# Kernel optimization log

Measured on AMD Instinct MI355X. Metric: run time of the kernel, lower is better.

The kernel has to match this reference:

```python
import jax, jax.numpy as jnp
import numpy as np

B = 2048          # batch
E = 32            # number of expert FCs (len(out_features_nested))
IN = 2048         # in_features
OUT = 1024        # out_features (uniform across experts)


def setup_inputs() -> dict:
    key = jax.random.key(0)
    k1, k2, k3, k4 = jax.random.split(key, 4)
    features = jax.random.normal(k1, (B, IN), dtype=jnp.float32)
    activated = jax.random.normal(k2, (B, E), dtype=jnp.float32)
    # Stacked per-expert Linear params: W[e] is [OUT, IN], b[e] is [OUT]
    W = jax.random.normal(k3, (E, OUT, IN), dtype=jnp.float32) * (1.0 / np.sqrt(IN))
    b = jax.random.normal(k4, (E, OUT), dtype=jnp.float32) * 0.01
    return {"features": features, "W": W, "b": b, "activated": activated, "top_k": 4}


def reference(features, W, b, activated, top_k):
    # Original: parent_indices = activated.argsort(dim=1)[:, :top_k]  (ascending!)
    idx = jnp.argsort(activated, axis=1)[:, :top_k]            # [B, K] int
    # Dense all-expert compute (grouped GEMM), then per-sample gather of the
    # top_k selected experts' outputs. Equivalent math to per-sample Linear calls.
    all_out = jnp.einsum('bi,eoi->beo', features, W) + b        # [B, E, OUT]
    out = jnp.take_along_axis(all_out, idx[:, :, None], axis=1)  # [B, K, OUT]
    return out
```

## Files before the change

### kernel.cpp

```cpp
#include <hip/hip_runtime.h>
#include <hip/hip_bf16.h>
#include <stdint.h>

#define B_N     2048
#define E_N     32
#define IN_N    2048
#define OUT_N   1024
#define TOPK    4

#define BM      128
#define BN      256
#define BK      32
#define NT      (OUT_N / BN)
#define NKT     (IN_N / BK)
#define THREADS 512
#define MAX_SLOTS 96
#define GRID_GEMM (MAX_SLOTS * NT)

#define WS_COUNTS 0
#define WS_NSLOTS 32
#define WS_DESC   64
#define WS_LISTS  256

typedef float  f32x4  __attribute__((ext_vector_type(4)));
typedef __bf16 bf16x8 __attribute__((ext_vector_type(8)));

union Pack8 { bf16x8 v; uint4 u; };

__device__ __forceinline__ uint4 pack8(f32x4 lo, f32x4 hi) {
  Pack8 p;
#pragma unroll
  for (int j = 0; j < 4; ++j) { p.v[j] = (__bf16)lo[j]; p.v[j + 4] = (__bf16)hi[j]; }
  return p.u;
}
__device__ __forceinline__ bf16x8 as_frag(uint4 u) { Pack8 p; p.u = u; return p.v; }

__global__ void k_zero(int* __restrict__ ws) {
  if (threadIdx.x < 64) ws[threadIdx.x] = 0;
}

__global__ void k_topk(const float* __restrict__ act, int* __restrict__ ws) {
  int b = blockIdx.x * blockDim.x + threadIdx.x;
  if (b >= B_N) return;
  float v[E_N];
  const float* a = act + (size_t)b * E_N;
#pragma unroll
  for (int e = 0; e < E_N; ++e) v[e] = a[e];
  unsigned chosen = 0;
#pragma unroll
  for (int k = 0; k < TOPK; ++k) {
    float mv = 3.4e38f; int mi = 0;
#pragma unroll
    for (int e = 0; e < E_N; ++e) {
      bool sel = (((chosen >> e) & 1u) == 0u) && (v[e] < mv);
      mv = sel ? v[e] : mv;
      mi = sel ? e : mi;
    }
    chosen |= (1u << mi);
    int pos = atomicAdd(&ws[WS_COUNTS + mi], 1);
    ws[WS_LISTS + mi * B_N + pos] = (b << 2) | k;
  }
}

__global__ void k_tiles(int* __restrict__ ws) {
  int e = threadIdx.x;
  int c = (e < E_N) ? ws[WS_COUNTS + e] : 0;
  int t = (c + BM - 1) / BM;
  int off = 0, tot = 0;
  for (int j = 0; j < E_N; ++j) {
    int tj = __shfl(t, j, 64);
    if (j < e) off += tj;
    tot += tj;
  }
  if (e < E_N) {
    for (int i = 0; i < t; ++i) ws[WS_DESC + off + i] = (e << 6) | i;
  }
  if (e == 0) ws[WS_NSLOTS] = tot;
}

__global__ __launch_bounds__(THREADS, 2)
void k_gemm(const float* __restrict__ feat, const float* __restrict__ Wm,
            const float* __restrict__ bias, const int* __restrict__ ws,
            float* __restrict__ out) {
  int p = blockIdx.x;
  int L = (p & 7) * (GRID_GEMM / 8) + (p >> 3);
  int nt   = L / MAX_SLOTS;
  int slot = L % MAX_SLOTS;
  if (slot >= ws[WS_NSLOTS]) return;
  int desc = ws[WS_DESC + slot];
  int e = desc >> 6, mt = desc & 63;
  int count = ws[WS_COUNTS + e];
  int m0 = mt * BM;

  __shared__ uint4 lds4[3072];
  __shared__ int gids[BM];

  int tid  = threadIdx.x;
  int lane = tid & 63;
  int wv   = tid >> 6;
  int wm   = wv >> 2;
  int wn   = wv & 3;

  int arow = tid >> 2, kq = tid & 3;
  int gid = -1;
  if (m0 + arow < count) gid = ws[WS_LISTS + e * B_N + m0 + arow];
  if (kq == 0) gids[arow] = gid;
  const float* aptr = feat + (size_t)(gid >> 2) * IN_N + kq * 8;
  int a_wi = arow * 4 + (kq ^ ((arow >> 1) & 3));

  int wrow = tid >> 2;
  const float* wptr = Wm + ((size_t)e * OUT_N + (size_t)(nt * BN + wrow)) * IN_N + kq * 8;
  int w_wi0 = 512 + wrow * 4 + (kq ^ ((wrow >> 1) & 3));
  int w_wi1 = w_wi0 + 512;

  int aidx[4], bidx[4];
#pragma unroll
  for (int mi = 0; mi < 4; ++mi) {
    int r = wm * 64 + mi * 16 + (lane & 15);
    aidx[mi] = r * 4 + ((lane >> 4) ^ ((r >> 1) & 3));
  }
#pragma unroll
  for (int ni = 0; ni < 4; ++ni) {
    int r = wn * 64 + ni * 16 + (lane & 15);
    bidx[ni] = 512 + r * 4 + ((lane >> 4) ^ ((r >> 1) & 3));
  }

  f32x4 ra[2], rw[4];
  const f32x4 zero4 = {0.f, 0.f, 0.f, 0.f};

#define LOAD_TILE(K0)                                                        \
  do {                                                                       \
    if (gid >= 0) {                                                          \
      ra[0] = *(const f32x4*)(aptr + (K0));                                  \
      ra[1] = *(const f32x4*)(aptr + (K0) + 4);                              \
    } else { ra[0] = zero4; ra[1] = zero4; }                                 \
    rw[0] = *(const f32x4*)(wptr + (K0));                                    \
    rw[1] = *(const f32x4*)(wptr + (K0) + 4);                                \
    rw[2] = *(const f32x4*)(wptr + (size_t)128 * IN_N + (K0));               \
    rw[3] = *(const f32x4*)(wptr + (size_t)128 * IN_N + (K0) + 4);           \
  } while (0)

#define WRITE_TILE(BUF)                                                      \
  do {                                                                       \
    lds4[(BUF) * 1536 + a_wi]  = pack8(ra[0], ra[1]);                        \
    lds4[(BUF) * 1536 + w_wi0] = pack8(rw[0], rw[1]);                        \
    lds4[(BUF) * 1536 + w_wi1] = pack8(rw[2], rw[3]);                        \
  } while (0)

  f32x4 acc[4][4] = {};

  LOAD_TILE(0);
  WRITE_TILE(0);
  __syncthreads();

  int cur = 0;
#pragma unroll 1
  for (int kt = 0; kt < NKT; ++kt) {
    bool pf = (kt + 1 < NKT);
    if (pf) LOAD_TILE((kt + 1) * BK);

    int base = cur * 1536;
    bf16x8 af[4], bfr[4];
#pragma unroll
    for (int mi = 0; mi < 4; ++mi) af[mi] = as_frag(lds4[base + aidx[mi]]);
#pragma unroll
    for (int ni = 0; ni < 4; ++ni) bfr[ni] = as_frag(lds4[base + bidx[ni]]);
#pragma unroll
    for (int mi = 0; mi < 4; ++mi)
#pragma unroll
      for (int ni = 0; ni < 4; ++ni)
        acc[mi][ni] = __builtin_amdgcn_mfma_f32_16x16x32_bf16(af[mi], bfr[ni], acc[mi][ni], 0, 0, 0);

    if (pf) WRITE_TILE(cur ^ 1);
    __syncthreads();
    cur ^= 1;
  }

  int grr[16];
#pragma unroll
  for (int mi = 0; mi < 4; ++mi)
#pragma unroll
    for (int j = 0; j < 4; ++j)
      grr[mi * 4 + j] = gids[wm * 64 + mi * 16 + (lane >> 4) * 4 + j];

#pragma unroll
  for (int ni = 0; ni < 4; ++ni) {
    int col = nt * BN + wn * 64 + ni * 16 + (lane & 15);
    float bs = bias[e * OUT_N + col];
#pragma unroll
    for (int mi = 0; mi < 4; ++mi) {
#pragma unroll
      for (int j = 0; j < 4; ++j) {
        int g = grr[mi * 4 + j];
        if (g >= 0) out[(size_t)g * OUT_N + col] = acc[mi][ni][j] + bs;
      }
    }
  }
}

extern "C" void kernel_launch(void* const* d_in, const int* in_sizes, int n_in,
                              void* d_out, int out_size, void* d_ws, size_t ws_size,
                              hipStream_t stream) {
  const float* feat = (const float*)d_in[0];
  const float* Wm   = (const float*)d_in[1];
  const float* bias = (const float*)d_in[2];
  const float* act  = (const float*)d_in[3];
  int*   ws  = (int*)d_ws;
  float* out = (float*)d_out;

  hipLaunchKernelGGL(k_zero,  dim3(1),          dim3(64),      0, stream, ws);
  hipLaunchKernelGGL(k_topk,  dim3(B_N / 256),  dim3(256),     0, stream, act, ws);
  hipLaunchKernelGGL(k_tiles, dim3(1),          dim3(64),      0, stream, ws);
  hipLaunchKernelGGL(k_gemm,  dim3(GRID_GEMM),  dim3(THREADS), 0, stream,
                     feat, Wm, bias, ws, out);
}
```

Baseline: 147.8 us.

## Reshape GEMM tile to 256x128 and regroup block-to-slot mapping

The output tile moves from 128x256 to 256x128 (rows by output columns), so each block covers more gathered token rows and fewer output columns. Each wave now holds an 8x2 MFMA accumulator grid, and gids are read from LDS during the epilogue instead of being cached in registers. The block index mapping is rewritten so that 8 consecutive slots share one output-column tile, which may improve L2 reuse of weights. Larger M tiles mean more padding waste on partially filled expert tiles, and the max-slot bound drops to 64.

```diff
diff --git a/kernel.cpp b/kernel.cpp
--- a/kernel.cpp
+++ b/kernel.cpp
@@ -8,13 +8,13 @@
 #define OUT_N   1024
 #define TOPK    4
 
-#define BM      128
-#define BN      256
+#define BM      256
+#define BN      128
 #define BK      32
 #define NT      (OUT_N / BN)
 #define NKT     (IN_N / BK)
 #define THREADS 512
-#define MAX_SLOTS 96
+#define MAX_SLOTS 64
 #define GRID_GEMM (MAX_SLOTS * NT)
 
 #define WS_COUNTS 0
@@ -83,9 +83,9 @@
             const float* __restrict__ bias, const int* __restrict__ ws,
             float* __restrict__ out) {
   int p = blockIdx.x;
-  int L = (p & 7) * (GRID_GEMM / 8) + (p >> 3);
-  int nt   = L / MAX_SLOTS;
-  int slot = L % MAX_SLOTS;
+  int j = p >> 3;
+  int slot = (p & 7) + ((j >> 3) << 3);
+  int nt   = j & 7;
   if (slot >= ws[WS_NSLOTS]) return;
   int desc = ws[WS_DESC + slot];
   int e = desc >> 6, mt = desc & 63;
@@ -101,31 +101,31 @@
   int wm   = wv >> 2;
   int wn   = wv & 3;
 
-  int arow = tid >> 2, kq = tid & 3;
+  int arow = tid >> 1, ah = tid & 1;
   int gid = -1;
   if (m0 + arow < count) gid = ws[WS_LISTS + e * B_N + m0 + arow];
-  if (kq == 0) gids[arow] = gid;
-  const float* aptr = feat + (size_t)(gid >> 2) * IN_N + kq * 8;
-  int a_wi = arow * 4 + (kq ^ ((arow >> 1) & 3));
-
-  int wrow = tid >> 2;
+  if (ah == 0) gids[arow] = gid;
+  const float* aptr = feat + (size_t)(gid >> 2) * IN_N + ah * 16;
+  int a_wi0 = arow * 4 + ((ah * 2)     ^ ((arow >> 1) & 3));
+  int a_wi1 = arow * 4 + ((ah * 2 + 1) ^ ((arow >> 1) & 3));
+
+  int wrow = tid >> 2, kq = tid & 3;
   const float* wptr = Wm + ((size_t)e * OUT_N + (size_t)(nt * BN + wrow)) * IN_N + kq * 8;
-  int w_wi0 = 512 + wrow * 4 + (kq ^ ((wrow >> 1) & 3));
-  int w_wi1 = w_wi0 + 512;
-
-  int aidx[4], bidx[4];
-#pragma unroll
-  for (int mi = 0; mi < 4; ++mi) {
-    int r = wm * 64 + mi * 16 + (lane & 15);
+  int w_wi = 1024 + wrow * 4 + (kq ^ ((wrow >> 1) & 3));
+
+  int aidx[8], bidx[2];
+#pragma unroll
+  for (int mi = 0; mi < 8; ++mi) {
+    int r = wm * 128 + mi * 16 + (lane & 15);
     aidx[mi] = r * 4 + ((lane >> 4) ^ ((r >> 1) & 3));
   }
 #pragma unroll
-  for (int ni = 0; ni < 4; ++ni) {
-    int r = wn * 64 + ni * 16 + (lane & 15);
-    bidx[ni] = 512 + r * 4 + ((lane >> 4) ^ ((r >> 1) & 3));
-  }
-
-  f32x4 ra[2], rw[4];
+  for (int ni = 0; ni < 2; ++ni) {
+    int r = wn * 32 + ni * 16 + (lane & 15);
+    bidx[ni] = 1024 + r * 4 + ((lane >> 4) ^ ((r >> 1) & 3));
+  }
+
+  f32x4 ra[4], rw[2];
   const f32x4 zero4 = {0.f, 0.f, 0.f, 0.f};
 
 #define LOAD_TILE(K0)                                                        \
@@ -133,21 +133,21 @@
     if (gid >= 0) {                                                          \
       ra[0] = *(const f32x4*)(aptr + (K0));                                  \
       ra[1] = *(const f32x4*)(aptr + (K0) + 4);                              \
-    } else { ra[0] = zero4; ra[1] = zero4; }                                 \
+      ra[2] = *(const f32x4*)(aptr + (K0) + 8);                              \
+      ra[3] = *(const f32x4*)(aptr + (K0) + 12);                             \
+    } else { ra[0] = zero4; ra[1] = zero4; ra[2] = zero4; ra[3] = zero4; }   \
     rw[0] = *(const f32x4*)(wptr + (K0));                                    \
     rw[1] = *(const f32x4*)(wptr + (K0) + 4);                                \
-    rw[2] = *(const f32x4*)(wptr + (size_t)128 * IN_N + (K0));               \
-    rw[3] = *(const f32x4*)(wptr + (size_t)128 * IN_N + (K0) + 4);           \
   } while (0)
 
 #define WRITE_TILE(BUF)                                                      \
   do {                                                                       \
-    lds4[(BUF) * 1536 + a_wi]  = pack8(ra[0], ra[1]);                        \
-    lds4[(BUF) * 1536 + w_wi0] = pack8(rw[0], rw[1]);                        \
-    lds4[(BUF) * 1536 + w_wi1] = pack8(rw[2], rw[3]);                        \
+    lds4[(BUF) * 1536 + a_wi0] = pack8(ra[0], ra[1]);                        \
+    lds4[(BUF) * 1536 + a_wi1] = pack8(ra[2], ra[3]);                        \
+    lds4[(BUF) * 1536 + w_wi]  = pack8(rw[0], rw[1]);                        \
   } while (0)
 
-  f32x4 acc[4][4] = {};
+  f32x4 acc[8][2] = {};
 
   LOAD_TILE(0);
   WRITE_TILE(0);
@@ -160,15 +160,15 @@
     if (pf) LOAD_TILE((kt + 1) * BK);
 
     int base = cur * 1536;
-    bf16x8 af[4], bfr[4];
-#pragma unroll
-    for (int mi = 0; mi < 4; ++mi) af[mi] = as_frag(lds4[base + aidx[mi]]);
-#pragma unroll
-    for (int ni = 0; ni < 4; ++ni) bfr[ni] = as_frag(lds4[base + bidx[ni]]);
-#pragma unroll
-    for (int mi = 0; mi < 4; ++mi)
-#pragma unroll
-      for (int ni = 0; ni < 4; ++ni)
+    bf16x8 af[8], bfr[2];
+#pragma unroll
+    for (int mi = 0; mi < 8; ++mi) af[mi] = as_frag(lds4[base + aidx[mi]]);
+#pragma unroll
+    for (int ni = 0; ni < 2; ++ni) bfr[ni] = as_frag(lds4[base + bidx[ni]]);
+#pragma unroll
+    for (int mi = 0; mi < 8; ++mi)
+#pragma unroll
+      for (int ni = 0; ni < 2; ++ni)
         acc[mi][ni] = __builtin_amdgcn_mfma_f32_16x16x32_bf16(af[mi], bfr[ni], acc[mi][ni], 0, 0, 0);
 
     if (pf) WRITE_TILE(cur ^ 1);
@@ -176,23 +176,16 @@
     cur ^= 1;
   }
 
-  int grr[16];
-#pragma unroll
-  for (int mi = 0; mi < 4; ++mi)
-#pragma unroll
-    for (int j = 0; j < 4; ++j)
-      grr[mi * 4 + j] = gids[wm * 64 + mi * 16 + (lane >> 4) * 4 + j];
-
-#pragma unroll
-  for (int ni = 0; ni < 4; ++ni) {
-    int col = nt * BN + wn * 64 + ni * 16 + (lane & 15);
+#pragma unroll
+  for (int ni = 0; ni < 2; ++ni) {
+    int col = nt * BN + wn * 32 + ni * 16 + (lane & 15);
     float bs = bias[e * OUT_N + col];
 #pragma unroll
-    for (int mi = 0; mi < 4; ++mi) {
-#pragma unroll
-      for (int j = 0; j < 4; ++j) {
-        int g = grr[mi * 4 + j];
-        if (g >= 0) out[(size_t)g * OUT_N + col] = acc[mi][ni][j] + bs;
+    for (int mi = 0; mi < 8; ++mi) {
+#pragma unroll
+      for (int j2 = 0; j2 < 4; ++j2) {
+        int g = gids[wm * 128 + mi * 16 + (lane >> 4) * 4 + j2];
+        if (g >= 0) out[(size_t)g * OUT_N + col] = acc[mi][ni][j2] + bs;
       }
     }
   }
```

New measurement: 170.9 us. 15.7% more time.

## Pre-convert features to bf16 and retile gather GEMM to 384x128 blocks

Applied to the files above, without the earlier changes.

Adds a pre-pass that converts the feature matrix to bf16 in workspace, so the GEMM loads half the activation bytes and skips per-tile conversion of A. The GEMM tile becomes 384 rows by 128 columns with 6x4 MFMA fragments per wave and occupancy 1, which raises reuse of each weight tile across more gathered rows and cuts the number of slots. Each expert is forced to at least one tile. The cost is an extra kernel launch and conversion pass, more padded rows in partially filled tiles, and lower occupancy.

```diff
diff --git a/kernel.cpp b/kernel.cpp
--- a/kernel.cpp
+++ b/kernel.cpp
@@ -8,19 +8,22 @@
 #define OUT_N   1024
 #define TOPK    4
 
-#define BM      128
-#define BN      256
+#define BM      384
+#define BN      128
 #define BK      32
-#define NT      (OUT_N / BN)
 #define NKT     (IN_N / BK)
 #define THREADS 512
-#define MAX_SLOTS 96
-#define GRID_GEMM (MAX_SLOTS * NT)
+#define MAX_SLOTS 56
+#define GRID_GEMM (MAX_SLOTS * 8)
+
+#define WBASE   1536
+#define BUFSTRIDE 2048
 
 #define WS_COUNTS 0
 #define WS_NSLOTS 32
 #define WS_DESC   64
 #define WS_LISTS  256
+#define FEATB_OFF 264192
 
 typedef float  f32x4  __attribute__((ext_vector_type(4)));
 typedef __bf16 bf16x8 __attribute__((ext_vector_type(8)));
@@ -37,6 +40,13 @@
 
 __global__ void k_zero(int* __restrict__ ws) {
   if (threadIdx.x < 64) ws[threadIdx.x] = 0;
+}
+
+__global__ void k_conv(const float* __restrict__ f, unsigned short* __restrict__ o) {
+  int i = (blockIdx.x * 256 + threadIdx.x) * 8;
+  f32x4 a = *(const f32x4*)(f + i);
+  f32x4 b = *(const f32x4*)(f + i + 4);
+  *(uint4*)(o + i) = pack8(a, b);
 }
 
 __global__ void k_topk(const float* __restrict__ act, int* __restrict__ ws) {
@@ -65,7 +75,8 @@
 __global__ void k_tiles(int* __restrict__ ws) {
   int e = threadIdx.x;
   int c = (e < E_N) ? ws[WS_COUNTS + e] : 0;
-  int t = (c + BM - 1) / BM;
+  int t = (e < E_N) ? ((c + BM - 1) / BM) : 0;
+  if (e < E_N && t < 1) t = 1;
   int off = 0, tot = 0;
   for (int j = 0; j < E_N; ++j) {
     int tj = __shfl(t, j, 64);
@@ -78,121 +89,119 @@
   if (e == 0) ws[WS_NSLOTS] = tot;
 }
 
-__global__ __launch_bounds__(THREADS, 2)
-void k_gemm(const float* __restrict__ feat, const float* __restrict__ Wm,
+__global__ __launch_bounds__(THREADS, 1)
+void k_gemm(const unsigned short* __restrict__ featb, const float* __restrict__ Wm,
             const float* __restrict__ bias, const int* __restrict__ ws,
             float* __restrict__ out) {
   int p = blockIdx.x;
-  int L = (p & 7) * (GRID_GEMM / 8) + (p >> 3);
-  int nt   = L / MAX_SLOTS;
-  int slot = L % MAX_SLOTS;
+  int slot = p >> 3;
+  int nt   = p & 7;
   if (slot >= ws[WS_NSLOTS]) return;
   int desc = ws[WS_DESC + slot];
   int e = desc >> 6, mt = desc & 63;
   int count = ws[WS_COUNTS + e];
   int m0 = mt * BM;
 
-  __shared__ uint4 lds4[3072];
+  __shared__ uint4 lds4[2 * BUFSTRIDE];
   __shared__ int gids[BM];
 
   int tid  = threadIdx.x;
   int lane = tid & 63;
   int wv   = tid >> 6;
-  int wm   = wv >> 2;
-  int wn   = wv & 3;
-
-  int arow = tid >> 2, kq = tid & 3;
-  int gid = -1;
-  if (m0 + arow < count) gid = ws[WS_LISTS + e * B_N + m0 + arow];
-  if (kq == 0) gids[arow] = gid;
-  const float* aptr = feat + (size_t)(gid >> 2) * IN_N + kq * 8;
-  int a_wi = arow * 4 + (kq ^ ((arow >> 1) & 3));
-
-  int wrow = tid >> 2;
-  const float* wptr = Wm + ((size_t)e * OUT_N + (size_t)(nt * BN + wrow)) * IN_N + kq * 8;
-  int w_wi0 = 512 + wrow * 4 + (kq ^ ((wrow >> 1) & 3));
-  int w_wi1 = w_wi0 + 512;
-
-  int aidx[4], bidx[4];
-#pragma unroll
-  for (int mi = 0; mi < 4; ++mi) {
-    int r = wm * 64 + mi * 16 + (lane & 15);
+  int wm   = wv >> 1;
+  int wn   = wv & 1;
+
+  if (tid < BM) {
+    int gr = m0 + tid;
+    gids[tid] = (gr < count) ? ws[WS_LISTS + e * B_N + gr] : -1;
+  }
+  __syncthreads();
+
+  int aphy[3];
+  const unsigned short* asrc[3];
+#pragma unroll
+  for (int i = 0; i < 3; ++i) {
+    int l = tid + 512 * i;
+    int row = l >> 2, seg = l & 3;
+    aphy[i] = row * 4 + (seg ^ ((row >> 1) & 3));
+    int g = gids[row];
+    g = (g >= 0) ? (g >> 2) : 0;
+    asrc[i] = featb + (size_t)g * IN_N + seg * 8;
+  }
+  int wrow = tid >> 2, wseg = tid & 3;
+  const float* wp = Wm + ((size_t)e * OUT_N + (size_t)(nt * BN + wrow)) * IN_N + wseg * 8;
+  int wphy = WBASE + wrow * 4 + (wseg ^ ((wrow >> 1) & 3));
+
+  int aidx[6], bidx[4];
+#pragma unroll
+  for (int mi = 0; mi < 6; ++mi) {
+    int r = wm * 96 + mi * 16 + (lane & 15);
     aidx[mi] = r * 4 + ((lane >> 4) ^ ((r >> 1) & 3));
   }
 #pragma unroll
   for (int ni = 0; ni < 4; ++ni) {
     int r = wn * 64 + ni * 16 + (lane & 15);
-    bidx[ni] = 512 + r * 4 + ((lane >> 4) ^ ((r >> 1) & 3));
-  }
-
-  f32x4 ra[2], rw[4];
-  const f32x4 zero4 = {0.f, 0.f, 0.f, 0.f};
-
-#define LOAD_TILE(K0)                                                        \
+    bidx[ni] = WBASE + r * 4 + ((lane >> 4) ^ ((r >> 1) & 3));
+  }
+
+  uint4 ra[3];
+  f32x4 rw[2];
+  f32x4 acc[6][4] = {};
+
+#define LOADK(KT)                                                            \
   do {                                                                       \
-    if (gid >= 0) {                                                          \
-      ra[0] = *(const f32x4*)(aptr + (K0));                                  \
-      ra[1] = *(const f32x4*)(aptr + (K0) + 4);                              \
-    } else { ra[0] = zero4; ra[1] = zero4; }                                 \
-    rw[0] = *(const f32x4*)(wptr + (K0));                                    \
-    rw[1] = *(const f32x4*)(wptr + (K0) + 4);                                \
-    rw[2] = *(const f32x4*)(wptr + (size_t)128 * IN_N + (K0));               \
-    rw[3] = *(const f32x4*)(wptr + (size_t)128 * IN_N + (K0) + 4);           \
+    ra[0] = *(const uint4*)(asrc[0] + (KT) * BK);                            \
+    ra[1] = *(const uint4*)(asrc[1] + (KT) * BK);                            \
+    ra[2] = *(const uint4*)(asrc[2] + (KT) * BK);                            \
+    rw[0] = *(const f32x4*)(wp + (size_t)(KT) * BK);                         \
+    rw[1] = *(const f32x4*)(wp + (size_t)(KT) * BK + 4);                     \
   } while (0)
 
-#define WRITE_TILE(BUF)                                                      \
+#define WRITEK(BUF)                                                          \
   do {                                                                       \
-    lds4[(BUF) * 1536 + a_wi]  = pack8(ra[0], ra[1]);                        \
-    lds4[(BUF) * 1536 + w_wi0] = pack8(rw[0], rw[1]);                        \
-    lds4[(BUF) * 1536 + w_wi1] = pack8(rw[2], rw[3]);                        \
+    lds4[(BUF) * BUFSTRIDE + aphy[0]] = ra[0];                               \
+    lds4[(BUF) * BUFSTRIDE + aphy[1]] = ra[1];                               \
+    lds4[(BUF) * BUFSTRIDE + aphy[2]] = ra[2];                               \
+    lds4[(BUF) * BUFSTRIDE + wphy]    = pack8(rw[0], rw[1]);                 \
   } while (0)
 
-  f32x4 acc[4][4] = {};
-
-  LOAD_TILE(0);
-  WRITE_TILE(0);
+  LOADK(0);
+  WRITEK(0);
   __syncthreads();
 
   int cur = 0;
 #pragma unroll 1
   for (int kt = 0; kt < NKT; ++kt) {
     bool pf = (kt + 1 < NKT);
-    if (pf) LOAD_TILE((kt + 1) * BK);
-
-    int base = cur * 1536;
-    bf16x8 af[4], bfr[4];
-#pragma unroll
-    for (int mi = 0; mi < 4; ++mi) af[mi] = as_frag(lds4[base + aidx[mi]]);
+    if (pf) LOADK(kt + 1);
+
+    int base = cur * BUFSTRIDE;
+    bf16x8 af[6], bfr[4];
+#pragma unroll
+    for (int mi = 0; mi < 6; ++mi) af[mi] = as_frag(lds4[base + aidx[mi]]);
 #pragma unroll
     for (int ni = 0; ni < 4; ++ni) bfr[ni] = as_frag(lds4[base + bidx[ni]]);
 #pragma unroll
-    for (int mi = 0; mi < 4; ++mi)
+    for (int mi = 0; mi < 6; ++mi)
 #pragma unroll
       for (int ni = 0; ni < 4; ++ni)
         acc[mi][ni] = __builtin_amdgcn_mfma_f32_16x16x32_bf16(af[mi], bfr[ni], acc[mi][ni], 0, 0, 0);
 
-    if (pf) WRITE_TILE(cur ^ 1);
+    if (pf) WRITEK(cur ^ 1);
     __syncthreads();
     cur ^= 1;
   }
-
-  int grr[16];
-#pragma unroll
-  for (int mi = 0; mi < 4; ++mi)
-#pragma unroll
-    for (int j = 0; j < 4; ++j)
-      grr[mi * 4 + j] = gids[wm * 64 + mi * 16 + (lane >> 4) * 4 + j];
 
 #pragma unroll
   for (int ni = 0; ni < 4; ++ni) {
     int col = nt * BN + wn * 64 + ni * 16 + (lane & 15);
     float bs = bias[e * OUT_N + col];
 #pragma unroll
-    for (int mi = 0; mi < 4; ++mi) {
-#pragma unroll
-      for (int j = 0; j < 4; ++j) {
-        int g = grr[mi * 4 + j];
-        if (g >= 0) out[(size_t)g * OUT_N + col] = acc[mi][ni][j] + bs;
+    for (int mi = 0; mi < 6; ++mi) {
+#pragma unroll
+      for (int j2 = 0; j2 < 4; ++j2) {
+        int g = gids[wm * 96 + mi * 16 + (lane >> 4) * 4 + j2];
+        if (g >= 0) out[(size_t)g * OUT_N + col] = acc[mi][ni][j2] + bs;
       }
     }
   }
@@ -206,11 +215,13 @@
   const float* bias = (const float*)d_in[2];
   const float* act  = (const float*)d_in[3];
   int*   ws  = (int*)d_ws;
+  unsigned short* featb = (unsigned short*)((char*)d_ws + FEATB_OFF);
   float* out = (float*)d_out;
 
-  hipLaunchKernelGGL(k_zero,  dim3(1),          dim3(64),      0, stream, ws);
-  hipLaunchKernelGGL(k_topk,  dim3(B_N / 256),  dim3(256),     0, stream, act, ws);
-  hipLaunchKernelGGL(k_tiles, dim3(1),          dim3(64),      0, stream, ws);
-  hipLaunchKernelGGL(k_gemm,  dim3(GRID_GEMM),  dim3(THREADS), 0, stream,
-                     feat, Wm, bias, ws, out);
-}
+  hipLaunchKernelGGL(k_zero,  dim3(1),                 dim3(64),      0, stream, ws);
+  hipLaunchKernelGGL(k_conv,  dim3(B_N * IN_N / 2048), dim3(256),     0, stream, feat, featb);
+  hipLaunchKernelGGL(k_topk,  dim3(B_N / 256),         dim3(256),     0, stream, act, ws);
+  hipLaunchKernelGGL(k_tiles, dim3(1),                 dim3(64),      0, stream, ws);
+  hipLaunchKernelGGL(k_gemm,  dim3(GRID_GEMM),         dim3(THREADS), 0, stream,
+                     featb, Wm, bias, ws, out);
+}
```

After: 225.7 us. +52.7%, slower.
